# Kernel optimization log

Hardware: AMD Instinct MI355X
Metric: run time of the kernel (lower is better)

Reference implementation:

```python
import jax, jax.numpy as jnp
import numpy as np

DIM = 768
HEADS = 12
HEAD_DIM = DIM // HEADS
WS = 14  # window size
MLP = 3072
EPS = 1e-6
SCALE = HEAD_DIM ** -0.5
B, H, W = 4, 64, 64


def setup_inputs() -> dict:
    key = jax.random.key(0)
    ks = jax.random.split(key, 8)
    s = 0.02
    f32 = jnp.float32
    return {
        "hidden_states": jax.random.normal(ks[0], (B, DIM, H, W), f32),
        "ln1_w": jnp.ones((DIM,), f32),
        "ln1_b": jnp.zeros((DIM,), f32),
        "qkv_w": jax.random.normal(ks[1], (DIM, 3 * DIM), f32) * s,
        "qkv_b": jnp.zeros((3 * DIM,), f32),
        "proj_w": jax.random.normal(ks[2], (DIM, DIM), f32) * s,
        "proj_b": jnp.zeros((DIM,), f32),
        "rel_pos_h": jax.random.normal(ks[3], (2 * WS - 1, HEAD_DIM), f32) * s,
        "rel_pos_w": jax.random.normal(ks[4], (2 * WS - 1, HEAD_DIM), f32) * s,
        "ln2_w": jnp.ones((DIM,), f32),
        "ln2_b": jnp.zeros((DIM,), f32),
        "fc1_w": jax.random.normal(ks[5], (DIM, MLP), f32) * s,
        "fc1_b": jnp.zeros((MLP,), f32),
        "fc2_w": jax.random.normal(ks[6], (MLP, DIM), f32) * s,
        "fc2_b": jnp.zeros((DIM,), f32),
    }


def _layer_norm(x, w, b):
    mu = jnp.mean(x, axis=-1, keepdims=True)
    var = jnp.mean(jnp.square(x - mu), axis=-1, keepdims=True)
    return (x - mu) * jax.lax.rsqrt(var + EPS) * w + b


def _get_rel_pos(size, rel_pos):
    # q_size == k_size == WS, rel_pos already has 2*WS-1 rows -> pure gather
    coords = jnp.arange(size)[:, None] - jnp.arange(size)[None, :] + (size - 1)
    return rel_pos[coords]  # (size, size, head_dim)


def _attention(x, qkv_w, qkv_b, proj_w, proj_b, rel_pos_h, rel_pos_w):
    nb, h, w, c = x.shape  # windows batch, WS, WS, DIM
    n = h * w
    qkv = x.reshape(nb, n, c) @ qkv_w + qkv_b  # (nb, n, 3*DIM)
    qkv = qkv.reshape(nb, n, 3, HEADS, HEAD_DIM).transpose(2, 0, 3, 1, 4)
    qkv = qkv.reshape(3, nb * HEADS, n, HEAD_DIM)
    q, k, v = qkv[0], qkv[1], qkv[2]
    attn = jnp.einsum('bqc,bkc->bqk', q * SCALE, k)  # (nb*HEADS, n, n)
    # decomposed relative position bias
    Rh = _get_rel_pos(h, rel_pos_h)  # (h, h, hd)
    Rw = _get_rel_pos(w, rel_pos_w)  # (w, w, hd)
    rq = q.reshape(-1, h, w, HEAD_DIM)
    rel_h = jnp.einsum('bhwc,hkc->bhwk', rq, Rh)
    rel_w = jnp.einsum('bhwc,wkc->bhwk', rq, Rw)
    attn = (attn.reshape(-1, h, w, h, w)
            + rel_h[:, :, :, :, None]
            + rel_w[:, :, :, None, :]).reshape(-1, n, n)
    attn = jax.nn.softmax(attn, axis=-1)
    out = attn @ v  # (nb*HEADS, n, hd)
    out = out.reshape(nb, HEADS, h, w, HEAD_DIM).transpose(0, 2, 3, 1, 4)
    out = out.reshape(nb, h, w, c)
    return out @ proj_w + proj_b


def reference(hidden_states, ln1_w, ln1_b, qkv_w, qkv_b, proj_w, proj_b,
              rel_pos_h, rel_pos_w, ln2_w, ln2_b, fc1_w, fc1_b, fc2_w, fc2_b):
    x = hidden_states.transpose(0, 2, 3, 1)  # NCHW -> NHWC
    b, h, w, c = x.shape
    shortcut = x
    x = _layer_norm(x, ln1_w, ln1_b)
    # window partition with padding
    ph = (WS - h % WS) % WS
    pw = (WS - w % WS) % WS
    x = jnp.pad(x, ((0, 0), (0, ph), (0, pw), (0, 0)))
    hp, wp = h + ph, w + pw
    x = x.reshape(b, hp // WS, WS, wp // WS, WS, c).transpose(0, 1, 3, 2, 4, 5)
    windows = x.reshape(-1, WS, WS, c)
    windows = _attention(windows, qkv_w, qkv_b, proj_w, proj_b, rel_pos_h, rel_pos_w)
    # window unpartition + crop
    x = windows.reshape(b, hp // WS, wp // WS, WS, WS, c).transpose(0, 1, 3, 2, 4, 5)
    x = x.reshape(b, hp, wp, c)[:, :h, :w, :]
    x = shortcut + x
    y = _layer_norm(x, ln2_w, ln2_b)
    y = jax.nn.gelu(y @ fc1_w + fc1_b, approximate=False) @ fc2_w + fc2_b
    x = x + y
    return x.transpose(0, 3, 1, 2)  # back to NCHW
```

## Files before the change

### kernel.cpp

```cpp
#include <hip/hip_runtime.h>
#include <cstdint>
#include <cstddef>

#define NIMG   4
#define GRIDSZ 64
#define CH     768
#define NHEAD  12
#define WSZ    14
#define NWINS  100
#define NTOK   196
#define MWIN   19600
#define MREAL  16384
#define MLPC   3072
#define QKSCALE 0.125f

#define KSTR 72
#define VSTR 216
#define PSTR 40

typedef unsigned short u16;
typedef __attribute__((ext_vector_type(8))) short bf16x8;
typedef __attribute__((ext_vector_type(4))) float f32x4;

__device__ __forceinline__ float b2f(u16 u) {
  uint32_t x = (uint32_t)u << 16; float f; __builtin_memcpy(&f, &x, 4); return f;
}
__device__ __forceinline__ u16 f2b(float f) {
  uint32_t x; __builtin_memcpy(&x, &f, 4);
  x += 0x7fffu + ((x >> 16) & 1u);
  return (u16)(x >> 16);
}

__device__ __forceinline__ float fast_gelu(float x) {
  float z  = x * 0.70710678118654752440f;
  float az = fabsf(z);
  float t  = 1.0f / (1.0f + 0.3275911f * az);
  float poly = ((((1.061405429f * t - 1.453152027f) * t + 1.421413741f) * t
                 - 0.284496736f) * t + 0.254829592f) * t;
  float e  = __expf(-az * az);
  float erfv = copysignf(1.0f - poly * e, z);
  return 0.5f * x * (1.0f + erfv);
}

__device__ __forceinline__ void gl_lds16(const u16* g, u16* l) {
  __builtin_amdgcn_global_load_lds(
      (const __attribute__((address_space(1))) unsigned int*)g,
      (__attribute__((address_space(3))) unsigned int*)l, 16, 0, 0);
}

__global__ __launch_bounds__(256) void k_nchw2nhwc(const float* __restrict__ in,
                                                   float* __restrict__ out) {
  __shared__ float tile[32][33];
  int b  = blockIdx.z;
  int g0 = blockIdx.x * 32;
  int c0 = blockIdx.y * 32;
  int tx = threadIdx.x, ty = threadIdx.y;
  const float* ip = in + (size_t)b * CH * 4096;
  float* op = out + (size_t)b * 4096 * CH;
#pragma unroll
  for (int k = 0; k < 32; k += 8)
    tile[ty + k][tx] = ip[(size_t)(c0 + ty + k) * 4096 + g0 + tx];
  __syncthreads();
#pragma unroll
  for (int k = 0; k < 32; k += 8)
    op[(size_t)(g0 + ty + k) * CH + c0 + tx] = tile[tx][ty + k];
}

__global__ __launch_bounds__(256) void k_nhwc2nchw(const float* __restrict__ in,
                                                   float* __restrict__ out) {
  __shared__ float tile[32][33];
  int b  = blockIdx.z;
  int g0 = blockIdx.x * 32;
  int c0 = blockIdx.y * 32;
  int tx = threadIdx.x, ty = threadIdx.y;
  const float* ip = in + (size_t)b * 4096 * CH;
  float* op = out + (size_t)b * CH * 4096;
#pragma unroll
  for (int k = 0; k < 32; k += 8)
    tile[ty + k][tx] = ip[(size_t)(g0 + ty + k) * CH + c0 + tx];
  __syncthreads();
#pragma unroll
  for (int k = 0; k < 32; k += 8)
    op[(size_t)(c0 + ty + k) * 4096 + g0 + tx] = tile[tx][ty + k];
}

__global__ __launch_bounds__(256) void k_wt(const float* __restrict__ in,
                                            u16* __restrict__ out,
                                            int K, int N) {
  __shared__ float t[32][33];
  int n0 = blockIdx.x * 32, k0 = blockIdx.y * 32;
  int tx = threadIdx.x, ty = threadIdx.y;
#pragma unroll
  for (int k = 0; k < 32; k += 8)
    t[ty + k][tx] = in[(size_t)(k0 + ty + k) * N + n0 + tx];
  __syncthreads();
#pragma unroll
  for (int k = 0; k < 32; k += 8)
    out[(size_t)(n0 + ty + k) * K + k0 + tx] = f2b(t[tx][ty + k]);
}

__device__ __forceinline__ float block_sum(float s, float* red) {
  __syncthreads();
#pragma unroll
  for (int off = 32; off > 0; off >>= 1) s += __shfl_down(s, off, 64);
  int wid = threadIdx.x >> 6, lane = threadIdx.x & 63;
  if (lane == 0) red[wid] = s;
  __syncthreads();
  return red[0] + red[1] + red[2] + red[3];
}

__global__ __launch_bounds__(256) void k_ln(const float* __restrict__ x,
                                            const float* __restrict__ wt,
                                            const float* __restrict__ bs,
                                            u16* __restrict__ y,
                                            int window_mode) {
  __shared__ float red[4];
  int row = blockIdx.x, tid = threadIdx.x;
  const float* xp = x + (size_t)row * CH;
  float v0 = xp[tid], v1 = xp[tid + 256], v2 = xp[tid + 512];
  float mu = block_sum(v0 + v1 + v2, red) * (1.0f / 768.0f);
  float d0 = v0 - mu, d1 = v1 - mu, d2 = v2 - mu;
  float var = block_sum(d0 * d0 + d1 * d1 + d2 * d2, red) * (1.0f / 768.0f);
  float rs = rsqrtf(var + 1e-6f);
  int orow = row;
  if (window_mode) {
    int b = row >> 12, hw = row & 4095;
    int h = hw >> 6, wc = hw & 63;
    orow = (b * 25 + (h / WSZ) * 5 + (wc / WSZ)) * NTOK + (h % WSZ) * WSZ + (wc % WSZ);
  }
  u16* yp = y + (size_t)orow * CH;
  yp[tid]       = f2b(d0 * rs * wt[tid]       + bs[tid]);
  yp[tid + 256] = f2b(d1 * rs * wt[tid + 256] + bs[tid + 256]);
  yp[tid + 512] = f2b(d2 * rs * wt[tid + 512] + bs[tid + 512]);
}

__global__ __launch_bounds__(256) void k_gemm_mfma(const u16* __restrict__ A,
                                                   const u16* __restrict__ BT,
                                                   const float* __restrict__ bias,
                                                   void* __restrict__ Cv,
                                                   u16* __restrict__ Vt,
                                                   int M, int N, int K,
                                                   int act, int mode, int row0) {
  __shared__ u16 As[3][128 * 32];
  __shared__ u16 Bs[3][128 * 32];
  int tid  = threadIdx.x;
  int lane = tid & 63, wave = tid >> 6;

  int gx   = gridDim.x;
  int nwg  = gx * gridDim.y;
  int orig = blockIdx.y * gx + blockIdx.x;
  int q = nwg >> 3, r = nwg & 7;
  int xcd = orig & 7, idx = orig >> 3;
  int wgid = (xcd < r ? xcd * (q + 1) : r * (q + 1) + (xcd - r) * q) + idx;
  int bn = wgid % gx, bm = wgid / gx;

  int wm = (wave & 1) * 64, wn = (wave >> 1) * 64;
  int l15 = lane & 15, quad = lane >> 4;

  f32x4 acc[4][4];
#pragma unroll
  for (int i = 0; i < 4; i++)
#pragma unroll
    for (int j = 0; j < 4; j++) acc[i][j] = (f32x4){0.f, 0.f, 0.f, 0.f};

  const u16* Atile = A + (size_t)bm * 128 * K;
  const u16* Btile = BT + (size_t)bn * 128 * K;

  int c0 = wave * 64 + lane;
  int c1 = c0 + 256;
  int ar0 = c0 >> 2, ao0 = (c0 & 3) * 8;
  int ar1 = c1 >> 2, ao1 = (c1 & 3) * 8;
  int lo0 = (wave * 64) * 8;
  int lo1 = (256 + wave * 64) * 8;

  const int nk = K >> 5;

#define STAGE_SLAB(slot, slab)                                          \
  do {                                                                  \
    int kk_ = (slab) << 5;                                              \
    gl_lds16(Atile + (size_t)ar0 * K + kk_ + ao0, &As[(slot)][lo0]);    \
    gl_lds16(Atile + (size_t)ar1 * K + kk_ + ao1, &As[(slot)][lo1]);    \
    gl_lds16(Btile + (size_t)ar0 * K + kk_ + ao0, &Bs[(slot)][lo0]);    \
    gl_lds16(Btile + (size_t)ar1 * K + kk_ + ao1, &Bs[(slot)][lo1]);    \
  } while (0)

#define COMPUTE_SLAB(slot)                                                   \
  do {                                                                       \
    bf16x8 af[4], bfv[4];                                                    \
    _Pragma("unroll")                                                        \
    for (int mi = 0; mi < 4; mi++)                                           \
      af[mi] = *(const bf16x8*)&As[(slot)][(size_t)(wm + mi * 16 + l15) * 32 \
                                           + quad * 8];                      \
    _Pragma("unroll")                                                        \
    for (int ni = 0; ni < 4; ni++)                                           \
      bfv[ni] = *(const bf16x8*)&Bs[(slot)][(size_t)(wn + ni * 16 + l15) * 32\
                                            + quad * 8];                     \
    _Pragma("unroll")                                                        \
    for (int mi = 0; mi < 4; mi++)                                           \
      _Pragma("unroll")                                                      \
      for (int ni = 0; ni < 4; ni++)                                         \
        acc[mi][ni] = __builtin_amdgcn_mfma_f32_16x16x32_bf16(               \
            bfv[ni], af[mi], acc[mi][ni], 0, 0, 0);                          \
  } while (0)

  STAGE_SLAB(0, 0);
  STAGE_SLAB(1, 1);

  int t = 0;
  for (; t < nk - 1; ++t) {
    asm volatile("s_waitcnt vmcnt(4)" ::: "memory");
    __builtin_amdgcn_s_barrier();
    __builtin_amdgcn_sched_barrier(0);
    if (t + 2 < nk) STAGE_SLAB((t + 2) % 3, t + 2);
    COMPUTE_SLAB(t % 3);
  }
  asm volatile("s_waitcnt vmcnt(0)" ::: "memory");
  __builtin_amdgcn_s_barrier();
  __builtin_amdgcn_sched_barrier(0);
  COMPUTE_SLAB(t % 3);

#undef STAGE_SLAB
#undef COMPUTE_SLAB

#pragma unroll
  for (int mi = 0; mi < 4; mi++) {
    int row = bm * 128 + wm + mi * 16 + l15;
    if (row >= M) continue;
    size_t gbase = 0;
    bool valid = true;
    int wloc = 0, tok = 0;
    if (mode == 2) {
      int rowa = row + row0;
      int widx = rowa / NTOK, tt = rowa % NTOK;
      int b = widx / 25, wq = widx % 25;
      int h = (wq / 5) * WSZ + tt / WSZ;
      int w = (wq % 5) * WSZ + tt % WSZ;
      valid = (h < GRIDSZ) && (w < GRIDSZ);
      gbase = valid ? ((size_t)((b * GRIDSZ + h) * GRIDSZ + w)) * CH : 0;
    }
    if (mode == 3) { wloc = row / NTOK; tok = row - wloc * NTOK; }
#pragma unroll
    for (int ni = 0; ni < 4; ni++) {
      int colb = bn * 128 + wn + ni * 16 + quad * 4;
      float4 b4 = *(const float4*)&bias[colb];
      float v[4] = {acc[mi][ni][0] + b4.x, acc[mi][ni][1] + b4.y,
                    acc[mi][ni][2] + b4.z, acc[mi][ni][3] + b4.w};
      if (act == 1) {
#pragma unroll
        for (int r2 = 0; r2 < 4; r2++) v[r2] = fast_gelu(v[r2]);
      }
      if (mode == 0) {
        ushort4 st = make_ushort4(f2b(v[0]), f2b(v[1]), f2b(v[2]), f2b(v[3]));
        *(ushort4*)((u16*)Cv + (size_t)row * N + colb) = st;
      } else if (mode == 1) {
        float4* p = (float4*)((float*)Cv + (size_t)row * N + colb);
        float4 o = *p;
        o.x += v[0]; o.y += v[1]; o.z += v[2]; o.w += v[3];
        *p = o;
      } else if (mode == 2) {
        if (valid) {
          float4* p = (float4*)((float*)Cv + gbase + colb);
          float4 o = *p;
          o.x += v[0]; o.y += v[1]; o.z += v[2]; o.w += v[3];
          *p = o;
        }
      } else {
        if (colb < 1536) {
          ushort4 st = make_ushort4(f2b(v[0]), f2b(v[1]), f2b(v[2]), f2b(v[3]));
          *(ushort4*)((u16*)Cv + (size_t)row * N + colb) = st;
        } else {
          int vv = colb - 1536, hd = vv >> 6, d = vv & 63;
          u16* vp = Vt + ((size_t)(wloc * NHEAD + hd) * 64 + d) * VSTR + tok;
#pragma unroll
          for (int r2 = 0; r2 < 4; r2++) vp[(size_t)r2 * VSTR] = f2b(v[r2]);
        }
      }
    }
  }
}

__global__ __launch_bounds__(256) void k_relbias(const u16* __restrict__ qkv,
                                                 const float* __restrict__ rel_h,
                                                 const float* __restrict__ rel_w,
                                                 u16* __restrict__ rhg,
                                                 u16* __restrict__ rwg,
                                                 int nrows) {
  int idx = blockIdx.x * 256 + threadIdx.x;
  if (idx >= nrows * NHEAD) return;
  int head = idx % NHEAD, row = idx / NHEAD;
  int wloc = row / NTOK, tok = row - wloc * NTOK;
  const u16* qp = qkv + (size_t)row * (3 * CH) + head * 64;
  float q[64];
#pragma unroll
  for (int d = 0; d < 64; d += 4) {
    ushort4 u4 = *(const ushort4*)(qp + d);
    q[d] = b2f(u4.x); q[d + 1] = b2f(u4.y); q[d + 2] = b2f(u4.z); q[d + 3] = b2f(u4.w);
  }
  int hq = tok / WSZ, wq = tok % WSZ;
  size_t obase = ((size_t)(wloc * NHEAD + head) * NTOK + tok) * 16;
  for (int kk = 0; kk < WSZ; kk++) {
    const float* rh = rel_h + (size_t)(hq - kk + WSZ - 1) * 64;
    const float* rw = rel_w + (size_t)(wq - kk + WSZ - 1) * 64;
    float sh = 0.0f, sw = 0.0f;
#pragma unroll
    for (int d = 0; d < 64; d++) { sh += q[d] * rh[d]; sw += q[d] * rw[d]; }
    rhg[obase + kk] = f2b(sh);
    rwg[obase + kk] = f2b(sw);
  }
}

__global__ __launch_bounds__(256) void k_attn_mfma(const u16* __restrict__ qkv,
                                                   const u16* __restrict__ Vt,
                                                   const u16* __restrict__ rhg,
                                                   const u16* __restrict__ rwg,
                                                   u16* __restrict__ out,
                                                   int win0) {
  __shared__ u16 Ks[NTOK * KSTR];
  __shared__ u16 Vs[64 * VSTR];
  __shared__ u16 Ps[4][16 * PSTR];
  int head = blockIdx.x, wloc = blockIdx.y;
  int tid = threadIdx.x, lane = tid & 63, wave = tid >> 6;
  int l15 = lane & 15, quad = lane >> 4;
  const u16* qbase = qkv + (size_t)wloc * NTOK * (3 * CH) + head * 64;

  for (int c = tid; c < NTOK * 8; c += 256) {
    int tok = c >> 3, part = c & 7;
    uint4 v = *(const uint4*)(qbase + (size_t)tok * (3 * CH) + CH + part * 8);
    *(uint4*)&Ks[tok * KSTR + part * 8] = v;
  }
  const u16* vb = Vt + (size_t)(wloc * NHEAD + head) * 64 * VSTR;
#pragma unroll
  for (int it = 0; it < 7; ++it) {
    int c = it * 256 + tid;
    if (c < 64 * VSTR / 8) gl_lds16(vb + (size_t)c * 8, Vs + ((size_t)it * 256 + wave * 64) * 8);
  }
  __syncthreads();

  const u16* rhp = rhg + ((size_t)(wloc * NHEAD + head) * NTOK) * 16;
  const u16* rwp = rwg + ((size_t)(wloc * NHEAD + head) * NTOK) * 16;
  int winabs = win0 + wloc;

  for (int t16 = wave; t16 < 13; t16 += 4) {
    int qtok = t16 * 16 + l15; if (qtok > NTOK - 1) qtok = NTOK - 1;
    bf16x8 aq0 = *(const bf16x8*)(qbase + (size_t)qtok * (3 * CH) + quad * 8);
    bf16x8 aq1 = *(const bf16x8*)(qbase + (size_t)qtok * (3 * CH) + 32 + quad * 8);

    f32x4 s[13];
#pragma unroll
    for (int ct = 0; ct < 13; ct++) s[ct] = (f32x4){0.f, 0.f, 0.f, 0.f};
#pragma unroll
    for (int ct = 0; ct < 13; ct++) {
      int ktok = ct * 16 + l15; if (ktok > NTOK - 1) ktok = NTOK - 1;
      bf16x8 bk0 = *(const bf16x8*)&Ks[ktok * KSTR + quad * 8];
      bf16x8 bk1 = *(const bf16x8*)&Ks[ktok * KSTR + 32 + quad * 8];
      s[ct] = __builtin_amdgcn_mfma_f32_16x16x32_bf16(aq0, bk0, s[ct], 0, 0, 0);
      s[ct] = __builtin_amdgcn_mfma_f32_16x16x32_bf16(aq1, bk1, s[ct], 0, 0, 0);
    }

    f32x4 o[4];
#pragma unroll
    for (int ni = 0; ni < 4; ni++) o[ni] = (f32x4){0.f, 0.f, 0.f, 0.f};
    float lsum[4] = {0.f, 0.f, 0.f, 0.f};
    int row0t = t16 * 16 + quad * 4;

#pragma unroll
    for (int cc = 0; cc < 7; ++cc) {
#pragma unroll
      for (int half = 0; half < 2; ++half) {
        int ct = cc * 2 + half;
        if (ct < 13) {
          int col = ct * 16 + l15;
          int jh = col / WSZ, jw = col - jh * WSZ;
          bool colok = col < NTOK;
#pragma unroll
          for (int r = 0; r < 4; r++) {
            int rowt = row0t + r; int rowc = rowt > NTOK - 1 ? NTOK - 1 : rowt;
            float bias = b2f(rhp[rowc * 16 + jh]) + b2f(rwp[rowc * 16 + jw]);
            float sv = s[ct][r] * QKSCALE + bias;
            float p = colok ? __expf(sv) : 0.f;
            lsum[r] += p;
            Ps[wave][(quad * 4 + r) * PSTR + half * 16 + l15] = f2b(p);
          }
        } else {
#pragma unroll
          for (int r = 0; r < 4; r++)
            Ps[wave][(quad * 4 + r) * PSTR + half * 16 + l15] = 0;
        }
      }
      bf16x8 pa = *(const bf16x8*)&Ps[wave][l15 * PSTR + quad * 8];
#pragma unroll
      for (int ni = 0; ni < 4; ni++) {
        bf16x8 bv = *(const bf16x8*)&Vs[(ni * 16 + l15) * VSTR + cc * 32 + quad * 8];
        o[ni] = __builtin_amdgcn_mfma_f32_16x16x32_bf16(pa, bv, o[ni], 0, 0, 0);
      }
    }

#pragma unroll
    for (int r = 0; r < 4; r++) {
#pragma unroll
      for (int m = 1; m < 16; m <<= 1) lsum[r] += __shfl_xor(lsum[r], m, 64);
    }

#pragma unroll
    for (int r = 0; r < 4; r++) {
      int rowt = row0t + r;
      if (rowt < NTOK) {
        float inv = 1.0f / lsum[r];
        u16* op = out + ((size_t)winabs * NTOK + rowt) * CH + head * 64;
#pragma unroll
        for (int ni = 0; ni < 4; ni++) op[ni * 16 + l15] = f2b(o[ni][r] * inv);
      }
    }
  }
}

extern "C" void kernel_launch(void* const* d_in, const int* in_sizes, int n_in,
                              void* d_out, int out_size, void* d_ws, size_t ws_size,
                              hipStream_t stream) {
  const float* hidden = (const float*)d_in[0];
  const float* ln1_w  = (const float*)d_in[1];
  const float* ln1_b  = (const float*)d_in[2];
  const float* qkv_w  = (const float*)d_in[3];
  const float* qkv_b  = (const float*)d_in[4];
  const float* proj_w = (const float*)d_in[5];
  const float* proj_b = (const float*)d_in[6];
  const float* rel_h  = (const float*)d_in[7];
  const float* rel_w  = (const float*)d_in[8];
  const float* ln2_w  = (const float*)d_in[9];
  const float* ln2_b  = (const float*)d_in[10];
  const float* fc1_w  = (const float*)d_in[11];
  const float* fc1_b  = (const float*)d_in[12];
  const float* fc2_w  = (const float*)d_in[13];
  const float* fc2_b  = (const float*)d_in[14];
  float* out = (float*)d_out;

  char* ws = (char*)d_ws;
  float* x_nhwc = (float*)ws;
  u16*   R1     = (u16*)(ws + 50331648);
  u16*   qkvT   = (u16*)(ws + 80437248);
  u16*   projT  = qkvT + (size_t)2304 * 768;
  u16*   fc1T   = projT + (size_t)768 * 768;
  u16*   fc2T   = fc1T + (size_t)3072 * 768;
  u16*   R2     = fc2T + (size_t)768 * 3072;
  size_t used   = (size_t)80437248 + 14155776;
  size_t r2e    = ws_size > used ? (ws_size - used) >> 1 : 0;

  const size_t PW_QKV = (size_t)NTOK * 3 * CH;
  const size_t PW_VT  = (size_t)NHEAD * 64 * VSTR;
  const size_t PW_RB  = (size_t)NHEAD * NTOK * 16;
  const size_t perwin = PW_QKV + PW_VT + 2 * PW_RB;
  size_t wc_s = r2e / perwin;
  int Wc = wc_s >= NWINS ? NWINS : (int)wc_s;
  if (Wc < 1) Wc = 1;
  size_t rc_s = (r2e / MLPC / 128) * 128;
  int Rc = rc_s >= MREAL ? MREAL : (int)rc_s;
  if (Rc < 128) Rc = 128;

  u16* Vt  = R2 + (size_t)Wc * PW_QKV;
  u16* rhg = Vt + (size_t)Wc * PW_VT;
  u16* rwg = rhg + (size_t)Wc * PW_RB;

  k_wt<<<dim3(72, 24), dim3(32, 8), 0, stream>>>(qkv_w, qkvT, CH, 3 * CH);
  k_wt<<<dim3(24, 24), dim3(32, 8), 0, stream>>>(proj_w, projT, CH, CH);
  k_wt<<<dim3(96, 24), dim3(32, 8), 0, stream>>>(fc1_w, fc1T, CH, MLPC);
  k_wt<<<dim3(24, 96), dim3(32, 8), 0, stream>>>(fc2_w, fc2T, MLPC, CH);

  hipMemsetAsync(R1, 0, (size_t)MWIN * CH * sizeof(u16), stream);

  k_nchw2nhwc<<<dim3(128, 24, NIMG), dim3(32, 8), 0, stream>>>(hidden, x_nhwc);
  k_ln<<<MREAL, 256, 0, stream>>>(x_nhwc, ln1_w, ln1_b, R1, 1);
  for (int w0 = 0; w0 < NWINS; w0 += Wc) {
    int wc = NWINS - w0 < Wc ? NWINS - w0 : Wc;
    int Mc = wc * NTOK;
    k_gemm_mfma<<<dim3(18, (Mc + 127) / 128), 256, 0, stream>>>(
        R1 + (size_t)w0 * NTOK * CH, qkvT, qkv_b, R2, Vt,
        Mc, 3 * CH, CH, 0, 3, 0);
    k_relbias<<<(Mc * NHEAD + 255) / 256, 256, 0, stream>>>(
        R2, rel_h, rel_w, rhg, rwg, Mc);
    k_attn_mfma<<<dim3(NHEAD, wc), 256, 0, stream>>>(
        R2, Vt, rhg, rwg, R1, w0);
  }
  k_gemm_mfma<<<dim3(6, (MWIN + 127) / 128), 256, 0, stream>>>(
      R1, projT, proj_b, x_nhwc, nullptr, MWIN, CH, CH, 0, 2, 0);
  k_ln<<<MREAL, 256, 0, stream>>>(x_nhwc, ln2_w, ln2_b, R1, 0);
  for (int r0 = 0; r0 < MREAL; r0 += Rc) {
    int rc = MREAL - r0 < Rc ? MREAL - r0 : Rc;
    k_gemm_mfma<<<dim3(24, (rc + 127) / 128), 256, 0, stream>>>(
        R1 + (size_t)r0 * CH, fc1T, fc1_b, R2, nullptr, rc, MLPC, CH, 1, 0, 0);
    k_gemm_mfma<<<dim3(6, (rc + 127) / 128), 256, 0, stream>>>(
        R2, fc2T, fc2_b, x_nhwc + (size_t)r0 * CH, nullptr, rc, CH, MLPC, 0, 1, 0);
  }
  k_nhwc2nchw<<<dim3(128, 24, NIMG), dim3(32, 8), 0, stream>>>(x_nhwc, out);
}
```

Baseline: 758.0 us.

## Enlarge GEMM M-tile to 256 and swizzle LDS layout against bank conflicts

Doubles the GEMM block tile from 128x128 to 256x128, so each wave computes 128x64 with 8x4 MFMA accumulators. This reuses each B slab across more rows and halves the number of workgroups. It also adds an XOR swizzle on the 16-byte chunk position, applied both to the global-to-LDS staging address and to the LDS fragment reads, to cut LDS bank conflicts. Costs are more accumulator registers per wave (launch_bounds now asks for 2 blocks), a larger LDS footprint, and fewer workgroups for small-N GEMMs like proj and fc2, which may underfill the CUs.

```diff
diff --git a/kernel.cpp b/kernel.cpp
--- a/kernel.cpp
+++ b/kernel.cpp
@@ -134,14 +134,14 @@
   yp[tid + 512] = f2b(d2 * rs * wt[tid + 512] + bs[tid + 512]);
 }
 
-__global__ __launch_bounds__(256) void k_gemm_mfma(const u16* __restrict__ A,
-                                                   const u16* __restrict__ BT,
-                                                   const float* __restrict__ bias,
-                                                   void* __restrict__ Cv,
-                                                   u16* __restrict__ Vt,
-                                                   int M, int N, int K,
-                                                   int act, int mode, int row0) {
-  __shared__ u16 As[3][128 * 32];
+__global__ __launch_bounds__(256, 2) void k_gemm_mfma(const u16* __restrict__ A,
+                                                      const u16* __restrict__ BT,
+                                                      const float* __restrict__ bias,
+                                                      void* __restrict__ Cv,
+                                                      u16* __restrict__ Vt,
+                                                      int M, int N, int K,
+                                                      int act, int mode, int row0) {
+  __shared__ u16 As[3][256 * 32];
   __shared__ u16 Bs[3][128 * 32];
   int tid  = threadIdx.x;
   int lane = tid & 63, wave = tid >> 6;
@@ -154,49 +154,53 @@
   int wgid = (xcd < r ? xcd * (q + 1) : r * (q + 1) + (xcd - r) * q) + idx;
   int bn = wgid % gx, bm = wgid / gx;
 
-  int wm = (wave & 1) * 64, wn = (wave >> 1) * 64;
+  int wm = (wave & 1) * 128, wn = (wave >> 1) * 64;
   int l15 = lane & 15, quad = lane >> 4;
-
-  f32x4 acc[4][4];
-#pragma unroll
-  for (int i = 0; i < 4; i++)
+  int xq = (quad ^ ((l15 >> 1) & 3)) * 8;
+
+  f32x4 acc[8][4];
+#pragma unroll
+  for (int i = 0; i < 8; i++)
 #pragma unroll
     for (int j = 0; j < 4; j++) acc[i][j] = (f32x4){0.f, 0.f, 0.f, 0.f};
 
-  const u16* Atile = A + (size_t)bm * 128 * K;
+  const u16* Atile = A + (size_t)bm * 256 * K;
   const u16* Btile = BT + (size_t)bn * 128 * K;
 
-  int c0 = wave * 64 + lane;
-  int c1 = c0 + 256;
-  int ar0 = c0 >> 2, ao0 = (c0 & 3) * 8;
-  int ar1 = c1 >> 2, ao1 = (c1 & 3) * 8;
-  int lo0 = (wave * 64) * 8;
-  int lo1 = (256 + wave * 64) * 8;
-
   const int nk = K >> 5;
 
-#define STAGE_SLAB(slot, slab)                                          \
-  do {                                                                  \
-    int kk_ = (slab) << 5;                                              \
-    gl_lds16(Atile + (size_t)ar0 * K + kk_ + ao0, &As[(slot)][lo0]);    \
-    gl_lds16(Atile + (size_t)ar1 * K + kk_ + ao1, &As[(slot)][lo1]);    \
-    gl_lds16(Btile + (size_t)ar0 * K + kk_ + ao0, &Bs[(slot)][lo0]);    \
-    gl_lds16(Btile + (size_t)ar1 * K + kk_ + ao1, &Bs[(slot)][lo1]);    \
+#define STAGE_SLAB(slot, slab)                                               \
+  do {                                                                       \
+    int kk_ = (slab) << 5;                                                   \
+    _Pragma("unroll")                                                        \
+    for (int i = 0; i < 4; ++i) {                                            \
+      int c_ = i * 256 + wave * 64 + lane;                                   \
+      int row_ = c_ >> 2, gs_ = (c_ & 3) ^ ((c_ >> 3) & 3);                  \
+      gl_lds16(Atile + (size_t)row_ * K + kk_ + gs_ * 8,                     \
+               &As[(slot)][(i * 256 + wave * 64) * 8]);                      \
+    }                                                                        \
+    _Pragma("unroll")                                                        \
+    for (int i = 0; i < 2; ++i) {                                            \
+      int c_ = i * 256 + wave * 64 + lane;                                   \
+      int row_ = c_ >> 2, gs_ = (c_ & 3) ^ ((c_ >> 3) & 3);                  \
+      gl_lds16(Btile + (size_t)row_ * K + kk_ + gs_ * 8,                     \
+               &Bs[(slot)][(i * 256 + wave * 64) * 8]);                      \
+    }                                                                        \
   } while (0)
 
 #define COMPUTE_SLAB(slot)                                                   \
   do {                                                                       \
-    bf16x8 af[4], bfv[4];                                                    \
+    bf16x8 af[8], bfv[4];                                                    \
     _Pragma("unroll")                                                        \
-    for (int mi = 0; mi < 4; mi++)                                           \
+    for (int mi = 0; mi < 8; mi++)                                           \
       af[mi] = *(const bf16x8*)&As[(slot)][(size_t)(wm + mi * 16 + l15) * 32 \
-                                           + quad * 8];                      \
+                                           + xq];                            \
     _Pragma("unroll")                                                        \
     for (int ni = 0; ni < 4; ni++)                                           \
       bfv[ni] = *(const bf16x8*)&Bs[(slot)][(size_t)(wn + ni * 16 + l15) * 32\
-                                            + quad * 8];                     \
+                                            + xq];                           \
     _Pragma("unroll")                                                        \
-    for (int mi = 0; mi < 4; mi++)                                           \
+    for (int mi = 0; mi < 8; mi++)                                           \
       _Pragma("unroll")                                                      \
       for (int ni = 0; ni < 4; ni++)                                         \
         acc[mi][ni] = __builtin_amdgcn_mfma_f32_16x16x32_bf16(               \
@@ -208,7 +212,7 @@
 
   int t = 0;
   for (; t < nk - 1; ++t) {
-    asm volatile("s_waitcnt vmcnt(4)" ::: "memory");
+    asm volatile("s_waitcnt vmcnt(6)" ::: "memory");
     __builtin_amdgcn_s_barrier();
     __builtin_amdgcn_sched_barrier(0);
     if (t + 2 < nk) STAGE_SLAB((t + 2) % 3, t + 2);
@@ -223,8 +227,8 @@
 #undef COMPUTE_SLAB
 
 #pragma unroll
-  for (int mi = 0; mi < 4; mi++) {
-    int row = bm * 128 + wm + mi * 16 + l15;
+  for (int mi = 0; mi < 8; mi++) {
+    int row = bm * 256 + wm + mi * 16 + l15;
     if (row >= M) continue;
     size_t gbase = 0;
     bool valid = true;
@@ -452,9 +456,9 @@
   size_t wc_s = r2e / perwin;
   int Wc = wc_s >= NWINS ? NWINS : (int)wc_s;
   if (Wc < 1) Wc = 1;
-  size_t rc_s = (r2e / MLPC / 128) * 128;
+  size_t rc_s = (r2e / MLPC / 256) * 256;
   int Rc = rc_s >= MREAL ? MREAL : (int)rc_s;
-  if (Rc < 128) Rc = 128;
+  if (Rc < 256) Rc = 256;
 
   u16* Vt  = R2 + (size_t)Wc * PW_QKV;
   u16* rhg = Vt + (size_t)Wc * PW_VT;
@@ -472,7 +476,7 @@
   for (int w0 = 0; w0 < NWINS; w0 += Wc) {
     int wc = NWINS - w0 < Wc ? NWINS - w0 : Wc;
     int Mc = wc * NTOK;
-    k_gemm_mfma<<<dim3(18, (Mc + 127) / 128), 256, 0, stream>>>(
+    k_gemm_mfma<<<dim3(18, (Mc + 255) / 256), 256, 0, stream>>>(
         R1 + (size_t)w0 * NTOK * CH, qkvT, qkv_b, R2, Vt,
         Mc, 3 * CH, CH, 0, 3, 0);
     k_relbias<<<(Mc * NHEAD + 255) / 256, 256, 0, stream>>>(
@@ -480,14 +484,14 @@
     k_attn_mfma<<<dim3(NHEAD, wc), 256, 0, stream>>>(
         R2, Vt, rhg, rwg, R1, w0);
   }
-  k_gemm_mfma<<<dim3(6, (MWIN + 127) / 128), 256, 0, stream>>>(
+  k_gemm_mfma<<<dim3(6, (MWIN + 255) / 256), 256, 0, stream>>>(
       R1, projT, proj_b, x_nhwc, nullptr, MWIN, CH, CH, 0, 2, 0);
   k_ln<<<MREAL, 256, 0, stream>>>(x_nhwc, ln2_w, ln2_b, R1, 0);
   for (int r0 = 0; r0 < MREAL; r0 += Rc) {
     int rc = MREAL - r0 < Rc ? MREAL - r0 : Rc;
-    k_gemm_mfma<<<dim3(24, (rc + 127) / 128), 256, 0, stream>>>(
+    k_gemm_mfma<<<dim3(24, (rc + 255) / 256), 256, 0, stream>>>(
         R1 + (size_t)r0 * CH, fc1T, fc1_b, R2, nullptr, rc, MLPC, CH, 1, 0, 0);
-    k_gemm_mfma<<<dim3(6, (rc + 127) / 128), 256, 0, stream>>>(
+    k_gemm_mfma<<<dim3(6, (rc + 255) / 256), 256, 0, stream>>>(
         R2, fc2T, fc2_b, x_nhwc + (size_t)r0 * CH, nullptr, rc, CH, MLPC, 0, 1, 0);
   }
   k_nhwc2nchw<<<dim3(128, 24, NIMG), dim3(32, 8), 0, stream>>>(x_nhwc, out);
```

After: 765.9 us. Within noise of the previous version (+1.0%).
